# Kernel tuning notes

Hardware: AMD Instinct MI355X
Metric: run time of the kernel (lower is better)

The kernel has to match this reference:

```python
import jax, jax.numpy as jnp
import numpy as np

B, S, D = 64, 1024, 128
EPS = 1e-5

def hardswish(x):
    return x * jnp.clip(x + 3.0, 0.0, 6.0) / 6.0

def setup_inputs() -> dict:
    key = jax.random.key(0)
    k1, k2, k3 = jax.random.split(key, 3)
    x = jax.random.normal(k1, (B, S, D), dtype=jnp.float32)
    ln_w = jnp.ones((S, D), dtype=jnp.float32)
    ln_b = jnp.zeros((S, D), dtype=jnp.float32)
    # U1[i]/U2[i] rows packed into lower-triangular (S,S); init ~ N(0,1)*0.01
    W1 = jax.random.normal(k2, (S, S), dtype=jnp.float32) * 0.01
    W2 = jax.random.normal(k3, (S, S), dtype=jnp.float32) * 0.01
    return {"x": x, "ln_w": ln_w, "ln_b": ln_b, "W1": W1, "W2": W2}

def reference(x, ln_w, ln_b, W1, W2):
    # LayerNorm over the last two dims (seq_len, feature_dim) jointly
    mu = jnp.mean(x, axis=(-2, -1), keepdims=True)
    var = jnp.mean(jnp.square(x - mu), axis=(-2, -1), keepdims=True)
    h = (x - mu) * jax.lax.rsqrt(var + EPS) * ln_w + ln_b
    # causal (lower-triangular) time mixing: u[:, t] = sum_{s<=t} W1[t, s] * h[:, s]
    mask = jnp.tril(jnp.ones((S, S), dtype=x.dtype))
    u = hardswish(jnp.einsum('ts,bsd->btd', W1 * mask, h))
    v = jnp.einsum('ts,bsd->btd', W2 * mask, u)
    return x + v
```

## Files before the change

### kernel.cpp

```cpp
#include <hip/hip_runtime.h>
#include <hip/hip_bf16.h>

#define NB 64
#define S_ 1024
#define D_ 128

typedef __attribute__((ext_vector_type(8))) short bf16x8;
typedef __attribute__((ext_vector_type(4))) float f32x4;
typedef __attribute__((ext_vector_type(4))) unsigned int u32x4;


__device__ __forceinline__ unsigned short f2bf(float f) {
  __hip_bfloat16 h = __float2bfloat16(f);
  return __builtin_bit_cast(unsigned short, h);
}

__device__ __forceinline__ void async_copy16(const void* g, void* l) {
  __builtin_amdgcn_global_load_lds(
      (const __attribute__((address_space(1))) unsigned int*)g,
      (__attribute__((address_space(3))) unsigned int*)l, 16, 0, 0);
}

__device__ __forceinline__ void store16_dev(void* p, bf16x8 v) {
  u32x4 d = __builtin_bit_cast(u32x4, v);
  asm volatile("global_store_dwordx4 %0, %1, off sc1" ::"v"(p), "v"(d)
               : "memory");
}

__device__ __forceinline__ void spin_mask(unsigned* p, unsigned need) {
  if (threadIdx.x == 0) {
    int guard = 0;
    while ((__hip_atomic_load(p, __ATOMIC_RELAXED, __HIP_MEMORY_SCOPE_AGENT) &
            need) != need) {
      __builtin_amdgcn_s_sleep(4);
      if (++guard > 400000) break;
    }
  }
  __syncthreads();
  asm volatile("" ::: "memory");
}

__device__ __forceinline__ void publish_bit(unsigned* p, unsigned bit) {
  asm volatile("s_waitcnt vmcnt(0)" ::: "memory");
  __syncthreads();
  if (threadIdx.x == 0)
    __hip_atomic_fetch_or(p, bit, __ATOMIC_RELAXED, __HIP_MEMORY_SCOPE_AGENT);
}

__global__ __launch_bounds__(256) void wpack_kernel(
    const float* __restrict__ W1, const float* __restrict__ W2,
    unsigned short* __restrict__ W1f, unsigned short* __restrict__ W2f,
    unsigned* __restrict__ stats) {
  const int blk = blockIdx.x;
  const int t = threadIdx.x;
  const int wave = t >> 6, lane = t & 63;
  const int quad = lane >> 4, l16 = lane & 15;
  if (blk == 0) {
#pragma unroll
    for (int i = 0; i < 8; ++i) stats[t + i * 256] = 0u;
  }
#pragma unroll
  for (int rep = 0; rep < 2; ++rep) {
    const int u = blk * 8 + wave * 2 + rep;
    const int f = u & 2047;
    const int p = f >> 5, c = f & 31;
    const int r = p * 16 + l16;
    const int k0 = c * 32 + quad * 8;
    const float* wsrc = ((u >> 11) ? W2 : W1) + (size_t)r * 1024 + k0;
    float4 a0 = ((const float4*)wsrc)[0];
    float4 a1 = ((const float4*)wsrc)[1];
    float av[8] = {a0.x, a0.y, a0.z, a0.w, a1.x, a1.y, a1.z, a1.w};
    bf16x8 o;
#pragma unroll
    for (int jj = 0; jj < 8; ++jj)
      o[jj] = (short)f2bf((k0 + jj <= r) ? av[jj] : 0.f);
    unsigned short* dstp = ((u >> 11) ? W2f : W1f) +
                           ((size_t)p * 32 + c) * 512 + lane * 8;
    *(bf16x8*)dstp = o;
  }
}

template <bool HSWISH>
__device__ __forceinline__ void gemm_phase(
    unsigned short* ldsA, const int b, const int mt,
    const unsigned short* __restrict__ Af, const unsigned short* __restrict__ Bf,
    unsigned short* __restrict__ Uf, const float* __restrict__ Xres,
    float* __restrict__ Out) {
  const int t = threadIdx.x;
  const int wave = t >> 6, lane = t & 63;
  const int quad = lane >> 4, l16 = lane & 15;
  const int row0 = mt * 64;

  const int cend = 2 * (mt + 1);
  const int npan = (cend + 7) >> 3;

  const unsigned short* Ab = Af + (size_t)mt * 4 * 32 * 512;
  const unsigned short* Bb = Bf + (size_t)b * (D_ * S_);

  f32x4 acc[4][2] = {};
  bf16x8 Bp[4][2];
#pragma unroll
  for (int g = 0; g < 4; ++g) {
    const int gg = (g < cend) ? g : 0;
#pragma unroll
    for (int jj = 0; jj < 2; ++jj)
      Bp[g][jj] = *(const bf16x8*)(Bb + ((size_t)(wave * 2 + jj) * 32 + gg) * 512 + lane * 8);
  }

  for (int p = 0; p < npan; ++p) {
    if (p) __syncthreads();
    const int rem = cend - p * 8;
#pragma unroll
    for (int jc = 0; jc < 8; ++jc) {
      const int flat16 = jc * 256 + t;
      const int iw = flat16 >> 9;
      const int cc = (flat16 >> 6) & 7;
      const int li = flat16 & 63;
      if (cc < rem)
        async_copy16(Ab + ((size_t)iw * 32 + p * 8 + cc) * 512 + li * 8,
                     ldsA + flat16 * 8);
    }
    __syncthreads();
#pragma unroll
    for (int c = 0; c < 8; ++c) {
      const int g = p * 8 + c;
      if (g < cend) {
        bf16x8 af[4];
#pragma unroll
        for (int i = 0; i < 4; ++i)
          af[i] = *(const bf16x8*)(ldsA + i * 4096 + c * 512 + lane * 8);
        __builtin_amdgcn_s_setprio(1);
#pragma unroll
        for (int i = 0; i < 4; ++i)
#pragma unroll
          for (int jj = 0; jj < 2; ++jj)
            acc[i][jj] = __builtin_amdgcn_mfma_f32_16x16x32_bf16(
                af[i], Bp[c & 3][jj], acc[i][jj], 0, 0, 0);
        __builtin_amdgcn_s_setprio(0);
        const int gn = (g + 4 < cend) ? (g + 4) : 0;
#pragma unroll
        for (int jj = 0; jj < 2; ++jj)
          Bp[c & 3][jj] = *(const bf16x8*)(
              Bb + ((size_t)(wave * 2 + jj) * 32 + gn) * 512 + lane * 8);
      }
    }
  }

  if (HSWISH) {
    __syncthreads();
    unsigned short* ldsT = ldsA;
#pragma unroll
    for (int i = 0; i < 4; ++i)
#pragma unroll
      for (int jj = 0; jj < 2; ++jj) {
        ushort4 pk;
        float v0 = acc[i][jj][0], v1 = acc[i][jj][1], v2 = acc[i][jj][2], v3 = acc[i][jj][3];
        pk.x = f2bf(v0 * fminf(fmaxf(v0 + 3.f, 0.f), 6.f) * (1.f / 6.f));
        pk.y = f2bf(v1 * fminf(fmaxf(v1 + 3.f, 0.f), 6.f) * (1.f / 6.f));
        pk.z = f2bf(v2 * fminf(fmaxf(v2 + 3.f, 0.f), 6.f) * (1.f / 6.f));
        pk.w = f2bf(v3 * fminf(fmaxf(v3 + 3.f, 0.f), 6.f) * (1.f / 6.f));
        const int n = wave * 32 + jj * 16 + l16;
        const int m0 = i * 16 + quad * 4;
        *(ushort4*)(ldsT + n * 72 + m0) = pk;
      }
    __syncthreads();
    unsigned short* gU = Uf + (size_t)b * (D_ * S_);
#pragma unroll
    for (int ff = 0; ff < 4; ++ff) {
      const int f = wave * 4 + ff;
      const int p2 = f >> 1, cl = f & 1;
      const int d = p2 * 16 + l16;
      const int tb = cl * 32 + quad * 8;
      bf16x8 v = *(const bf16x8*)(ldsT + d * 72 + tb);
      store16_dev(gU + ((size_t)p2 * 32 + mt * 2 + cl) * 512 + lane * 8, v);
    }
  } else {
    float* gO = Out + (size_t)b * S_ * D_;
    const float* gX = Xres + (size_t)b * S_ * D_;
#pragma unroll
    for (int i = 0; i < 4; ++i) {
      const int mrow0 = row0 + i * 16 + quad * 4;
#pragma unroll
      for (int jj = 0; jj < 2; ++jj) {
        const int col = wave * 32 + jj * 16 + l16;
#pragma unroll
        for (int r = 0; r < 4; ++r) {
          const int addr = (mrow0 + r) * D_ + col;
          gO[addr] = gX[addr] + acc[i][jj][r];
        }
      }
    }
  }
}

__global__ __launch_bounds__(256, 4) void mega_kernel(
    const float* __restrict__ x, const float* __restrict__ ln_w,
    const float* __restrict__ ln_b, const unsigned short* __restrict__ W1f,
    const unsigned short* __restrict__ W2f, float* __restrict__ stats,
    unsigned short* __restrict__ hTf, unsigned short* __restrict__ uTf,
    float* __restrict__ out) {
  __shared__ __align__(16) unsigned short smem[16384];

  const int bi = blockIdx.x;
  const int xcd = bi & 7;
  const int slot = bi >> 3;
  const int b = xcd * 8 + (slot & 7);
  const int j = slot >> 3;
  const int mt = (j < 8) ? j : (j ^ 3);

  const int t = threadIdx.x;
  const int wave = t >> 6, lane = t & 63;
  const int quad = lane >> 4, l16 = lane & 15;

  float* sb = stats + (size_t)b * 32;
  unsigned* cntp = (unsigned*)sb + 2;
  unsigned* hmp = (unsigned*)sb + 4;
  unsigned* ump = (unsigned*)sb + 6;

  float2* w4 = (float2*)(smem + 8448);
  float* mr = (float*)(smem + 8464);

  const float4* xb = (const float4*)(x + ((size_t)b * S_ + mt * 64) * D_);
  {
    float s = 0.f, q = 0.f;
#pragma unroll
    for (int i = 0; i < 8; ++i) {
      float4 v = xb[i * 256 + t];
      s += v.x + v.y + v.z + v.w;
      q += v.x * v.x + v.y * v.y + v.z * v.z + v.w * v.w;
    }
#pragma unroll
    for (int o = 32; o > 0; o >>= 1) {
      s += __shfl_down(s, o, 64);
      q += __shfl_down(q, o, 64);
    }
    if (lane == 0) w4[wave] = make_float2(s, q);
  }
  __syncthreads();
  if (t == 0) {
    float ss = 0.f, qq = 0.f;
#pragma unroll
    for (int i = 0; i < 4; ++i) { ss += w4[i].x; qq += w4[i].y; }
    float o1 = __hip_atomic_fetch_add(sb + 0, ss, __ATOMIC_RELAXED,
                                      __HIP_MEMORY_SCOPE_AGENT);
    float o2 = __hip_atomic_fetch_add(sb + 1, qq, __ATOMIC_RELAXED,
                                      __HIP_MEMORY_SCOPE_AGENT);
    asm volatile("" ::"v"(o1), "v"(o2));
    __hip_atomic_fetch_add(cntp, 1u, __ATOMIC_RELAXED,
                           __HIP_MEMORY_SCOPE_AGENT);
    int guard = 0;
    while (__hip_atomic_load(cntp, __ATOMIC_RELAXED,
                             __HIP_MEMORY_SCOPE_AGENT) < 16u) {
      __builtin_amdgcn_s_sleep(4);
      if (++guard > 400000) break;
    }
    float s1 = __hip_atomic_load(sb + 0, __ATOMIC_RELAXED,
                                 __HIP_MEMORY_SCOPE_AGENT);
    float s2 = __hip_atomic_load(sb + 1, __ATOMIC_RELAXED,
                                 __HIP_MEMORY_SCOPE_AGENT);
    const float inv = 1.0f / (S_ * D_);
    const float mu = s1 * inv;
    mr[0] = mu;
    mr[1] = rsqrtf(s2 * inv - mu * mu + 1e-5f);
  }
  __syncthreads();
  const float mu = mr[0];
  const float rs = mr[1];

  {
    unsigned short* lds = smem;
    const float4* wb = (const float4*)(ln_w + (size_t)(mt * 64) * D_);
    const float4* bv4 = (const float4*)(ln_b + (size_t)(mt * 64) * D_);
#pragma unroll
    for (int r = 0; r < 8; ++r) {
      const int f = r * 256 + t;
      const int srow = f >> 5;
      const int c4 = f & 31;
      float4 xv = xb[f];
      float4 wv = wb[f];
      float4 bvv = bv4[f];
      ushort4 o;
      o.x = f2bf((xv.x - mu) * rs * wv.x + bvv.x);
      o.y = f2bf((xv.y - mu) * rs * wv.y + bvv.y);
      o.z = f2bf((xv.z - mu) * rs * wv.z + bvv.z);
      o.w = f2bf((xv.w - mu) * rs * wv.w + bvv.w);
      *(ushort4*)(lds + srow * 132 + c4 * 4) = o;
    }
    __syncthreads();
    unsigned short* outp = hTf + (size_t)b * (D_ * S_);
    const int cg0 = mt * 2;
#pragma unroll
    for (int ff = 0; ff < 4; ++ff) {
      const int f = wave * 4 + ff;
      const int p = f >> 1, cl = f & 1;
      const int d = p * 16 + l16;
      const int sbase = cl * 32 + quad * 8;
      bf16x8 v;
#pragma unroll
      for (int jj = 0; jj < 8; ++jj)
        v[jj] = (short)lds[(sbase + jj) * 132 + d];
      store16_dev(outp + ((size_t)p * 32 + cg0 + cl) * 512 + lane * 8, v);
    }
  }
  publish_bit(hmp, 1u << mt);

  spin_mask(hmp, (2u << mt) - 1);
  gemm_phase<true>(smem, b, mt, W1f, hTf, uTf, nullptr, nullptr);
  publish_bit(ump, 1u << mt);

  spin_mask(ump, (2u << mt) - 1);
  gemm_phase<false>(smem, b, mt, W2f, uTf, nullptr, x, out);
}

extern "C" void kernel_launch(void* const* d_in, const int* in_sizes, int n_in,
                              void* d_out, int out_size, void* d_ws, size_t ws_size,
                              hipStream_t stream) {
  const float* x = (const float*)d_in[0];
  const float* ln_w = (const float*)d_in[1];
  const float* ln_b = (const float*)d_in[2];
  const float* W1 = (const float*)d_in[3];
  const float* W2 = (const float*)d_in[4];
  float* out = (float*)d_out;

  char* ws = (char*)d_ws;
  float* stats = (float*)ws;
  unsigned short* W1f = (unsigned short*)(ws + 16384);
  unsigned short* W2f = W1f + (size_t)S_ * S_;
  unsigned short* hTf = W2f + (size_t)S_ * S_;
  unsigned short* uTf = hTf + (size_t)NB * D_ * S_;

  wpack_kernel<<<512, 256, 0, stream>>>(W1, W2, W1f, W2f, (unsigned*)stats);
  mega_kernel<<<1024, 256, 0, stream>>>(x, ln_w, ln_b, W1f, W2f, stats,
                                        hTf, uTf, out);
}
```

Measured before the change: 132.0 us.

## Fuse weight packing into mega kernel and reverse second-GEMM tile order

```diff
diff --git a/kernel.cpp b/kernel.cpp
--- a/kernel.cpp
+++ b/kernel.cpp
@@ -40,6 +40,19 @@
   asm volatile("" ::: "memory");
 }
 
+__device__ __forceinline__ void spin_cnt(unsigned* p, unsigned need) {
+  if (threadIdx.x == 0) {
+    int guard = 0;
+    while (__hip_atomic_load(p, __ATOMIC_RELAXED, __HIP_MEMORY_SCOPE_AGENT) <
+           need) {
+      __builtin_amdgcn_s_sleep(4);
+      if (++guard > 400000) break;
+    }
+  }
+  __syncthreads();
+  asm volatile("" ::: "memory");
+}
+
 __device__ __forceinline__ void publish_bit(unsigned* p, unsigned bit) {
   asm volatile("s_waitcnt vmcnt(0)" ::: "memory");
   __syncthreads();
@@ -47,37 +60,9 @@
     __hip_atomic_fetch_or(p, bit, __ATOMIC_RELAXED, __HIP_MEMORY_SCOPE_AGENT);
 }
 
-__global__ __launch_bounds__(256) void wpack_kernel(
-    const float* __restrict__ W1, const float* __restrict__ W2,
-    unsigned short* __restrict__ W1f, unsigned short* __restrict__ W2f,
-    unsigned* __restrict__ stats) {
-  const int blk = blockIdx.x;
-  const int t = threadIdx.x;
-  const int wave = t >> 6, lane = t & 63;
-  const int quad = lane >> 4, l16 = lane & 15;
-  if (blk == 0) {
-#pragma unroll
-    for (int i = 0; i < 8; ++i) stats[t + i * 256] = 0u;
-  }
-#pragma unroll
-  for (int rep = 0; rep < 2; ++rep) {
-    const int u = blk * 8 + wave * 2 + rep;
-    const int f = u & 2047;
-    const int p = f >> 5, c = f & 31;
-    const int r = p * 16 + l16;
-    const int k0 = c * 32 + quad * 8;
-    const float* wsrc = ((u >> 11) ? W2 : W1) + (size_t)r * 1024 + k0;
-    float4 a0 = ((const float4*)wsrc)[0];
-    float4 a1 = ((const float4*)wsrc)[1];
-    float av[8] = {a0.x, a0.y, a0.z, a0.w, a1.x, a1.y, a1.z, a1.w};
-    bf16x8 o;
-#pragma unroll
-    for (int jj = 0; jj < 8; ++jj)
-      o[jj] = (short)f2bf((k0 + jj <= r) ? av[jj] : 0.f);
-    unsigned short* dstp = ((u >> 11) ? W2f : W1f) +
-                           ((size_t)p * 32 + c) * 512 + lane * 8;
-    *(bf16x8*)dstp = o;
-  }
+__global__ __launch_bounds__(256) void init_stats(unsigned* __restrict__ c) {
+#pragma unroll
+  for (int i = 0; i < 8; ++i) c[threadIdx.x + i * 256] = 0u;
 }
 
 template <bool HSWISH>
@@ -195,8 +180,9 @@
 
 __global__ __launch_bounds__(256, 4) void mega_kernel(
     const float* __restrict__ x, const float* __restrict__ ln_w,
-    const float* __restrict__ ln_b, const unsigned short* __restrict__ W1f,
-    const unsigned short* __restrict__ W2f, float* __restrict__ stats,
+    const float* __restrict__ ln_b, const float* __restrict__ W1,
+    const float* __restrict__ W2, float* __restrict__ stats,
+    unsigned short* __restrict__ W1f, unsigned short* __restrict__ W2f,
     unsigned short* __restrict__ hTf, unsigned short* __restrict__ uTf,
     float* __restrict__ out) {
   __shared__ __align__(16) unsigned short smem[16384];
@@ -216,16 +202,19 @@
   unsigned* cntp = (unsigned*)sb + 2;
   unsigned* hmp = (unsigned*)sb + 4;
   unsigned* ump = (unsigned*)sb + 6;
+  unsigned* wcnt = (unsigned*)stats + 16;
 
   float2* w4 = (float2*)(smem + 8448);
   float* mr = (float*)(smem + 8464);
 
   const float4* xb = (const float4*)(x + ((size_t)b * S_ + mt * 64) * D_);
+  float4 xv[8];
   {
     float s = 0.f, q = 0.f;
 #pragma unroll
     for (int i = 0; i < 8; ++i) {
       float4 v = xb[i * 256 + t];
+      xv[i] = v;
       s += v.x + v.y + v.z + v.w;
       q += v.x * v.x + v.y * v.y + v.z * v.z + v.w * v.w;
     }
@@ -248,6 +237,31 @@
     asm volatile("" ::"v"(o1), "v"(o2));
     __hip_atomic_fetch_add(cntp, 1u, __ATOMIC_RELAXED,
                            __HIP_MEMORY_SCOPE_AGENT);
+  }
+
+  {
+    const int u = bi * 4 + wave;
+    const int f = u & 2047;
+    const int p = f >> 5, c = f & 31;
+    const int r = p * 16 + l16;
+    const int k0 = c * 32 + quad * 8;
+    const float* wsrc = ((u >> 11) ? W2 : W1) + (size_t)r * 1024 + k0;
+    float4 a0 = ((const float4*)wsrc)[0];
+    float4 a1 = ((const float4*)wsrc)[1];
+    float av[8] = {a0.x, a0.y, a0.z, a0.w, a1.x, a1.y, a1.z, a1.w};
+    bf16x8 o;
+#pragma unroll
+    for (int jj = 0; jj < 8; ++jj)
+      o[jj] = (short)f2bf((k0 + jj <= r) ? av[jj] : 0.f);
+    unsigned short* dstp = ((u >> 11) ? W2f : W1f) +
+                           ((size_t)p * 32 + c) * 512 + lane * 8;
+    store16_dev(dstp, o);
+  }
+  asm volatile("s_waitcnt vmcnt(0)" ::: "memory");
+  __syncthreads();
+  if (t == 0) {
+    __hip_atomic_fetch_add(wcnt, 1u, __ATOMIC_RELAXED,
+                           __HIP_MEMORY_SCOPE_AGENT);
     int guard = 0;
     while (__hip_atomic_load(cntp, __ATOMIC_RELAXED,
                              __HIP_MEMORY_SCOPE_AGENT) < 16u) {
@@ -276,14 +290,13 @@
       const int f = r * 256 + t;
       const int srow = f >> 5;
       const int c4 = f & 31;
-      float4 xv = xb[f];
       float4 wv = wb[f];
       float4 bvv = bv4[f];
       ushort4 o;
-      o.x = f2bf((xv.x - mu) * rs * wv.x + bvv.x);
-      o.y = f2bf((xv.y - mu) * rs * wv.y + bvv.y);
-      o.z = f2bf((xv.z - mu) * rs * wv.z + bvv.z);
-      o.w = f2bf((xv.w - mu) * rs * wv.w + bvv.w);
+      o.x = f2bf((xv[r].x - mu) * rs * wv.x + bvv.x);
+      o.y = f2bf((xv[r].y - mu) * rs * wv.y + bvv.y);
+      o.z = f2bf((xv[r].z - mu) * rs * wv.z + bvv.z);
+      o.w = f2bf((xv[r].w - mu) * rs * wv.w + bvv.w);
       *(ushort4*)(lds + srow * 132 + c4 * 4) = o;
     }
     __syncthreads();
@@ -304,12 +317,14 @@
   }
   publish_bit(hmp, 1u << mt);
 
+  spin_cnt(wcnt, 1024);
   spin_mask(hmp, (2u << mt) - 1);
   gemm_phase<true>(smem, b, mt, W1f, hTf, uTf, nullptr, nullptr);
   publish_bit(ump, 1u << mt);
 
-  spin_mask(ump, (2u << mt) - 1);
-  gemm_phase<false>(smem, b, mt, W2f, uTf, nullptr, x, out);
+  const int mt2 = 15 - mt;
+  spin_mask(ump, (2u << mt2) - 1);
+  gemm_phase<false>(smem, b, mt2, W2f, uTf, nullptr, x, out);
 }
 
 extern "C" void kernel_launch(void* const* d_in, const int* in_sizes, int n_in,
@@ -329,7 +344,7 @@
   unsigned short* hTf = W2f + (size_t)S_ * S_;
   unsigned short* uTf = hTf + (size_t)NB * D_ * S_;
 
-  wpack_kernel<<<512, 256, 0, stream>>>(W1, W2, W1f, W2f, (unsigned*)stats);
-  mega_kernel<<<1024, 256, 0, stream>>>(x, ln_w, ln_b, W1f, W2f, stats,
-                                        hTf, uTf, out);
-}
+  init_stats<<<1, 256, 0, stream>>>((unsigned*)stats);
+  mega_kernel<<<1024, 256, 0, stream>>>(x, ln_w, ln_b, W1, W2, stats,
+                                        W1f, W2f, hTf, uTf, out);
+}
```

Result: slower. 146.9 us (+11.3%).
